# Optimization experiments

Measured on AMD Instinct MI355X. Metric: run time of the kernel, lower is better.

Reference implementation:

```python
import jax, jax.numpy as jnp
import numpy as np
from jax import lax

HIDDEN = 128
HEADS = 2
SR = 4
EPS = 1e-5


def _rope(x, fr, fi):
    # x: (B, h, S, d) ; fr, fi: (S, d//2) broadcast as (1,1,S,c)
    B, H, S, D = x.shape
    x2 = x.reshape(B, H, S, D // 2, 2)
    xr, xi = x2[..., 0], x2[..., 1]
    fr = fr[None, None, :, :]
    fi = fi[None, None, :, :]
    out_r = xr * fr - xi * fi
    out_i = xr * fi + xi * fr
    return jnp.stack([out_r, out_i], axis=-1).reshape(B, H, S, D)


def _layernorm(x, g, b):
    mu = jnp.mean(x, axis=-1, keepdims=True)
    var = jnp.mean(jnp.square(x - mu), axis=-1, keepdims=True)
    return (x - mu) * lax.rsqrt(var + EPS) * g + b


def setup_inputs() -> dict:
    key = jax.random.key(0)
    ks = jax.random.split(key, 12)
    B, S, C = 2, 16384, HIDDEN
    s = 0.02
    return {
        "hidden_states": jax.random.normal(ks[0], (B, S, C), jnp.float32),
        "freqs_cis": jax.random.normal(ks[1], (S, C // HEADS // 2, 2), jnp.float32),
        "Wq": jax.random.normal(ks[2], (C, C), jnp.float32) * s,
        "bq": jnp.zeros((C,), jnp.float32),
        "Wk": jax.random.normal(ks[3], (C, C), jnp.float32) * s,
        "bk": jnp.zeros((C,), jnp.float32),
        "Wv": jax.random.normal(ks[4], (C, C), jnp.float32) * s,
        "bv": jnp.zeros((C,), jnp.float32),
        "W_sr": jax.random.normal(ks[5], (C, C, SR, SR), jnp.float32) * s,  # (O,I,kh,kw)
        "b_sr": jnp.zeros((C,), jnp.float32),
        "ln_g": jnp.ones((C,), jnp.float32),
        "ln_b": jnp.zeros((C,), jnp.float32),
        "height": 128,
        "width": 128,
    }


def reference(hidden_states, freqs_cis, Wq, bq, Wk, bk, Wv, bv, W_sr, b_sr, ln_g, ln_b, height, width):
    B, S, C = hidden_states.shape
    h, d = HEADS, C // HEADS
    c = d // 2

    # query projection on full-resolution tokens
    q = (hidden_states @ Wq.T + bq).reshape(B, S, h, d).transpose(0, 2, 1, 3)  # (B,h,S,d)

    # sequence reduction: conv stride=kernel=SR on (B,C,H,W), then layernorm
    x_img = hidden_states.transpose(0, 2, 1).reshape(B, C, height, width)
    xr = lax.conv_general_dilated(x_img, W_sr, window_strides=(SR, SR), padding="VALID")
    xr = xr + b_sr[None, :, None, None]
    Sk = (height // SR) * (width // SR)
    xr = xr.reshape(B, C, Sk).transpose(0, 2, 1)  # (B, S', C)
    xr = _layernorm(xr, ln_g, ln_b)

    k = (xr @ Wk.T + bk).reshape(B, Sk, h, d).transpose(0, 2, 1, 3)
    v = (xr @ Wv.T + bv).reshape(B, Sk, h, d).transpose(0, 2, 1, 3)

    # RoPE: queries use full freqs; keys use sr-pooled (block-mean) freqs
    fr, fi = freqs_cis[..., 0], freqs_cis[..., 1]  # (S, c)
    q = _rope(q, fr, fi)

    fr_img = fr.reshape(height // SR, SR, width // SR, SR, c).mean(axis=(1, 3))
    fi_img = fi.reshape(height // SR, SR, width // SR, SR, c).mean(axis=(1, 3))
    fr_k = fr_img.reshape(Sk, c)
    fi_k = fi_img.reshape(Sk, c)
    k = _rope(k, fr_k, fi_k)

    scores = jnp.einsum("bhqd,bhkd->bhqk", q, k) / jnp.sqrt(jnp.float32(d))
    probs = jax.nn.softmax(scores, axis=-1)
    ctx = jnp.einsum("bhqk,bhkd->bhqd", probs, v)
    return ctx.transpose(0, 2, 1, 3).reshape(B, S, C)
```

## Files before the change

### kernel.cpp

```cpp
#include <hip/hip_runtime.h>
#include <math.h>

#define B_   2
#define S_   16384
#define SK_  1024
#define IMW_ 128
#define EPS_ 1e-5f

typedef __attribute__((ext_vector_type(8))) short short8v;
typedef __attribute__((ext_vector_type(4))) short short4v;
typedef __attribute__((ext_vector_type(4))) float f32x4;

__device__ __forceinline__ ushort f2bfu(float x) {
    uint u = __float_as_uint(x);
    u += 0x7fffu + ((u >> 16) & 1u);
    return (ushort)(u >> 16);
}
__device__ __forceinline__ uint cvtpk(float a, float b) {
    uint r;
    asm("v_cvt_pk_bf16_f32 %0, %1, %2" : "=v"(r) : "v"(a), "v"(b));
    return r;
}
__device__ __forceinline__ short8v pack8(float4 a, float4 b) {
    union { uint4 u; short8v s; } c;
    c.u = make_uint4(cvtpk(a.x, a.y), cvtpk(a.z, a.w), cvtpk(b.x, b.y), cvtpk(b.z, b.w));
    return c.s;
}

__global__ __launch_bounds__(256) void k_prep(
    const float* __restrict__ Wsr, const float* __restrict__ Wq,
    const float* __restrict__ Wk,  const float* __restrict__ Wv,
    const float* __restrict__ fc,
    ushort* __restrict__ Wsrb, ushort* __restrict__ Wqb,
    ushort* __restrict__ Wkb,  ushort* __restrict__ Wvb,
    float* __restrict__ frk, float* __restrict__ fik)
{
    const int blk = blockIdx.x, t = threadIdx.x;
    if (blk < 64) {
        int i = blk * 256 + t;
        int co = i >> 7, ci = i & 127;
        const float* src = Wsr + (size_t)i * 16;
        float4 v0 = *(const float4*)(src);
        float4 v1 = *(const float4*)(src + 4);
        float4 v2 = *(const float4*)(src + 8);
        float4 v3 = *(const float4*)(src + 12);
        float vv[16] = {v0.x, v0.y, v0.z, v0.w, v1.x, v1.y, v1.z, v1.w,
                        v2.x, v2.y, v2.z, v2.w, v3.x, v3.y, v3.z, v3.w};
        ushort* dst = Wsrb + (size_t)co * 2048 + ci;
        #pragma unroll
        for (int tap = 0; tap < 16; ++tap) dst[tap * 128] = f2bfu(vv[tap]);
    } else if (blk < 88) {
        int seg = (blk - 64) >> 3;
        const float* src = (seg == 0) ? Wq : (seg == 1) ? Wk : Wv;
        ushort* dst = (seg == 0) ? Wqb : (seg == 1) ? Wkb : Wvb;
        int i = ((blk - 64) & 7) * 2048 + t * 8;
        float4 a = *(const float4*)(src + i);
        float4 b = *(const float4*)(src + i + 4);
        *(uint4*)(dst + i) = make_uint4(cvtpk(a.x, a.y), cvtpk(a.z, a.w),
                                        cvtpk(b.x, b.y), cvtpk(b.z, b.w));
    } else {
        int idx = (blk - 88) * 256 + t;
        int c = idx & 31, kk = idx >> 5;
        int y = kk >> 5, x = kk & 31;
        float sr = 0.f, si = 0.f;
        #pragma unroll
        for (int i1 = 0; i1 < 4; ++i1)
            #pragma unroll
            for (int i3 = 0; i3 < 4; ++i3) {
                int s = (4 * y + i1) * IMW_ + 4 * x + i3;
                sr += fc[s * 64 + 2 * c];
                si += fc[s * 64 + 2 * c + 1];
            }
        frk[idx] = sr * 0.0625f;
        fik[idx] = si * 0.0625f;
    }
}

__global__ __launch_bounds__(512) void k_conv(
    const float* __restrict__ hid, const ushort* __restrict__ Wsrb,
    float* __restrict__ partial)
{
    const int t = threadIdx.x;
    const int lane = t & 63, w = t >> 6;
    const int g = lane >> 4, ln = lane & 15;
    const int b = blockIdx.x >> 6, pt = blockIdx.x & 63;
    const int pos = pt * 16 + ln;
    const int y = pos >> 5, x = pos & 31;

    f32x4 acc[8];
    #pragma unroll
    for (int mt = 0; mt < 8; ++mt)
        #pragma unroll
        for (int r = 0; r < 4; ++r) acc[mt][r] = 0.f;

    #pragma unroll
    for (int st = 0; st < 8; ++st) {
        const int tap = 2 * w + (st >> 2);
        const int ci0 = (st & 3) * 32;
        const int ky = tap >> 2, kx = tap & 3;
        const float* hp = hid + ((size_t)b * S_ + (4 * y + ky) * IMW_ + 4 * x + kx) * 128 + ci0 + 8 * g;
        short8v xf = pack8(*(const float4*)hp, *(const float4*)(hp + 4));
        #pragma unroll
        for (int mt = 0; mt < 8; ++mt) {
            short8v wf = *(const short8v*)(Wsrb + (size_t)(16 * mt + ln) * 2048 + tap * 128 + ci0 + 8 * g);
            acc[mt] = __builtin_amdgcn_mfma_f32_16x16x32_bf16(wf, xf, acc[mt], 0, 0, 0);
        }
    }
    float* dst = partial + ((size_t)w * 2048 + b * 1024 + pos) * 128 + 4 * g;
    #pragma unroll
    for (int mt = 0; mt < 8; ++mt)
        *(float4*)(dst + 16 * mt) = make_float4(acc[mt][0], acc[mt][1], acc[mt][2], acc[mt][3]);
}

__global__ __launch_bounds__(256) void k_lnkv(
    const float* __restrict__ partial, const float* __restrict__ bsr,
    const float* __restrict__ lng, const float* __restrict__ lnb,
    const float* __restrict__ FRK, const float* __restrict__ FIK,
    const ushort* __restrict__ Wkb, const ushort* __restrict__ Wvb,
    const float* __restrict__ bk, const float* __restrict__ bv,
    ushort* __restrict__ Kb, ushort* __restrict__ VTb)
{
    __shared__ ushort sXb[16][128];
    const int t = threadIdx.x;
    const int lane = t & 63, w = t >> 6;
    const int g = lane >> 4, ln = lane & 15;
    const int b = blockIdx.x >> 6;
    const int row0 = blockIdx.x * 16;
    const int pos0 = (blockIdx.x & 63) * 16;

    {
        const int row = t >> 4, j0 = (t & 15) * 8;
        float4 b0 = *(const float4*)(bsr + j0);
        float4 b1 = *(const float4*)(bsr + j0 + 4);
        float v[8] = {b0.x, b0.y, b0.z, b0.w, b1.x, b1.y, b1.z, b1.w};
        #pragma unroll
        for (int s = 0; s < 8; ++s) {
            const float* pp = partial + ((size_t)s * 2048 + row0 + row) * 128 + j0;
            float4 a = *(const float4*)pp;
            float4 c = *(const float4*)(pp + 4);
            v[0] += a.x; v[1] += a.y; v[2] += a.z; v[3] += a.w;
            v[4] += c.x; v[5] += c.y; v[6] += c.z; v[7] += c.w;
        }
        float s = v[0] + v[1] + v[2] + v[3] + v[4] + v[5] + v[6] + v[7];
        #pragma unroll
        for (int m = 1; m < 16; m <<= 1) s += __shfl_xor(s, m, 64);
        float mu = s * (1.0f / 128.0f);
        float d[8], vs = 0.f;
        #pragma unroll
        for (int j = 0; j < 8; ++j) { d[j] = v[j] - mu; vs += d[j] * d[j]; }
        #pragma unroll
        for (int m = 1; m < 16; m <<= 1) vs += __shfl_xor(vs, m, 64);
        float rstd = rsqrtf(vs * (1.0f / 128.0f) + EPS_);
        float4 g0 = *(const float4*)(lng + j0);
        float4 g1 = *(const float4*)(lng + j0 + 4);
        float4 c0 = *(const float4*)(lnb + j0);
        float4 c1 = *(const float4*)(lnb + j0 + 4);
        float o[8];
        o[0] = d[0] * rstd * g0.x + c0.x; o[1] = d[1] * rstd * g0.y + c0.y;
        o[2] = d[2] * rstd * g0.z + c0.z; o[3] = d[3] * rstd * g0.w + c0.w;
        o[4] = d[4] * rstd * g1.x + c1.x; o[5] = d[5] * rstd * g1.y + c1.y;
        o[6] = d[6] * rstd * g1.z + c1.z; o[7] = d[7] * rstd * g1.w + c1.w;
        *(uint4*)&sXb[row][j0 ^ ((row & 7) << 3)] =
            make_uint4(cvtpk(o[0], o[1]), cvtpk(o[2], o[3]),
                       cvtpk(o[4], o[5]), cvtpk(o[6], o[7]));
    }
    __syncthreads();

    short8v xn[4];
    #pragma unroll
    for (int ks = 0; ks < 4; ++ks)
        xn[ks] = *(const short8v*)&sXb[ln][(32 * ks + 8 * g) ^ ((ln & 7) << 3)];

    const int h = w & 1;
    const ushort* Wb = (w < 2) ? Wkb : Wvb;
    f32x4 acc2[4];
    #pragma unroll
    for (int mt = 0; mt < 4; ++mt)
        #pragma unroll
        for (int r = 0; r < 4; ++r) acc2[mt][r] = 0.f;
    #pragma unroll
    for (int mt = 0; mt < 4; ++mt)
        #pragma unroll
        for (int ks = 0; ks < 4; ++ks) {
            short8v wf = *(const short8v*)(Wb + (size_t)(64 * h + 16 * mt + ln) * 128 + 32 * ks + 8 * g);
            acc2[mt] = __builtin_amdgcn_mfma_f32_16x16x32_bf16(wf, xn[ks], acc2[mt], 0, 0, 0);
        }

    const int posg = pos0 + ln;
    const int bh = b * 2 + h;
    if (w < 2) {
        #pragma unroll
        for (int mt = 0; mt < 4; ++mt) {
            int col0 = 16 * mt + 4 * g;
            float4 bkv = *(const float4*)(bk + 64 * h + col0);
            float a0 = acc2[mt][0] + bkv.x, a1 = acc2[mt][1] + bkv.y;
            float a2 = acc2[mt][2] + bkv.z, a3 = acc2[mt][3] + bkv.w;
            float2 frv = *(const float2*)(FRK + (size_t)posg * 32 + (col0 >> 1));
            float2 fiv = *(const float2*)(FIK + (size_t)posg * 32 + (col0 >> 1));
            float o0 = a0 * frv.x - a1 * fiv.x;
            float o1 = a0 * fiv.x + a1 * frv.x;
            float o2 = a2 * frv.y - a3 * fiv.y;
            float o3 = a2 * fiv.y + a3 * frv.y;
            *(uint2*)(Kb + ((size_t)bh * SK_ + posg) * 64 + col0) =
                make_uint2(cvtpk(o0, o1), cvtpk(o2, o3));
        }
    } else {
        #pragma unroll
        for (int mt = 0; mt < 4; ++mt) {
            int col0 = 16 * mt + 4 * g;
            float4 bvv = *(const float4*)(bv + 64 * h + col0);
            #pragma unroll
            for (int r = 0; r < 4; ++r)
                VTb[((size_t)bh * 64 + col0 + r) * SK_ + posg] =
                    f2bfu(acc2[mt][r] + (&bvv.x)[r]);
        }
    }
}

__global__ __launch_bounds__(256) void k_attn(
    const float* __restrict__ hid, const ushort* __restrict__ Wqb,
    const float* __restrict__ bq, const float* __restrict__ fc,
    const ushort* __restrict__ Kb, const ushort* __restrict__ VTb,
    float* __restrict__ out)
{
    __shared__ ushort sK[2][64][64];
    __shared__ ushort sV[2][64][64];

    const int t = threadIdx.x;
    const int lane = t & 63, w = t >> 6;
    const int g = lane >> 4, ln = lane & 15;
    const int sbid = (blockIdx.x & 7) * 64 + (blockIdx.x >> 3);
    const int bh = sbid >> 7;
    const int q0b = (sbid & 127) * 128;
    const int b = bh >> 1, h = bh & 1;

    char* sQt = (char*)&sK[0][0][0];

    {
        f32x4 qa[2][4];
        #pragma unroll
        for (int qt = 0; qt < 2; ++qt)
            #pragma unroll
            for (int mt = 0; mt < 4; ++mt)
                #pragma unroll
                for (int r = 0; r < 4; ++r) qa[qt][mt][r] = 0.f;

        #pragma unroll
        for (int ks = 0; ks < 4; ++ks) {
            short8v xf[2];
            #pragma unroll
            for (int qt = 0; qt < 2; ++qt) {
                const float* hp = hid + ((size_t)b * S_ + q0b + w * 32 + 16 * qt + ln) * 128 + 32 * ks + 8 * g;
                xf[qt] = pack8(*(const float4*)hp, *(const float4*)(hp + 4));
            }
            #pragma unroll
            for (int mt = 0; mt < 4; ++mt) {
                short8v wf = *(const short8v*)(Wqb + (size_t)(64 * h + 16 * mt + ln) * 128 + 32 * ks + 8 * g);
                qa[0][mt] = __builtin_amdgcn_mfma_f32_16x16x32_bf16(wf, xf[0], qa[0][mt], 0, 0, 0);
                qa[1][mt] = __builtin_amdgcn_mfma_f32_16x16x32_bf16(wf, xf[1], qa[1][mt], 0, 0, 0);
            }
        }
        const float scale = 0.18033688011112042f;
        #pragma unroll
        for (int qt = 0; qt < 2; ++qt) {
            const int r = w * 32 + 16 * qt + ln;
            const int pos = q0b + r;
            #pragma unroll
            for (int mt = 0; mt < 4; ++mt) {
                int col0 = 16 * mt + 4 * g;
                float4 fv = *(const float4*)(fc + (size_t)pos * 64 + col0);
                float4 bqv = *(const float4*)(bq + 64 * h + col0);
                float a0 = qa[qt][mt][0] + bqv.x, a1 = qa[qt][mt][1] + bqv.y;
                float a2 = qa[qt][mt][2] + bqv.z, a3 = qa[qt][mt][3] + bqv.w;
                float o0 = (a0 * fv.x - a1 * fv.y) * scale;
                float o1 = (a0 * fv.y + a1 * fv.x) * scale;
                float o2 = (a2 * fv.z - a3 * fv.w) * scale;
                float o3 = (a2 * fv.w + a3 * fv.z) * scale;
                int cb = ((col0 >> 3) ^ (r & 7));
                *(uint2*)(sQt + r * 128 + cb * 16 + (g & 1) * 8) =
                    make_uint2(cvtpk(o0, o1), cvtpk(o2, o3));
            }
        }
    }
    short8v qf[2][2];
    #pragma unroll
    for (int qt = 0; qt < 2; ++qt)
        #pragma unroll
        for (int ks = 0; ks < 2; ++ks) {
            const int r = w * 32 + 16 * qt + ln;
            qf[qt][ks] = *(const short8v*)(sQt + r * 128 + (((4 * ks + g) ^ (r & 7)) * 16));
        }
    __syncthreads();

    const int r0 = t >> 3,        m0 = t & 7;
    const int r1 = (t + 256) >> 3, m1 = t & 7;
    const int vA0 = 32 * (m0 >> 2) + 4 * (m0 & 3);
    const int vA1 = 32 * (m1 >> 2) + 4 * (m1 & 3);
    const ushort* kgB = Kb  + (size_t)bh * SK_ * 64;
    const ushort* vgB = VTb + (size_t)bh * 64 * SK_;

    uint4 kb0, kb1, vb0, vb1;
    auto loadCh = [&](int ch) {
        const ushort* kp = kgB + (size_t)ch * 4096;
        kb0 = *(const uint4*)(kp + r0 * 64 + m0 * 8);
        kb1 = *(const uint4*)(kp + r1 * 64 + m1 * 8);
        const ushort* vp = vgB + ch * 64;
        uint2 a0 = *(const uint2*)(vp + (size_t)r0 * SK_ + vA0);
        uint2 b0 = *(const uint2*)(vp + (size_t)r0 * SK_ + vA0 + 16);
        uint2 a1 = *(const uint2*)(vp + (size_t)r1 * SK_ + vA1);
        uint2 b1 = *(const uint2*)(vp + (size_t)r1 * SK_ + vA1 + 16);
        vb0 = make_uint4(a0.x, a0.y, b0.x, b0.y);
        vb1 = make_uint4(a1.x, a1.y, b1.x, b1.y);
    };
    auto writeBuf = [&](int p) {
        char* kd = (char*)&sK[p][0][0];
        char* vd = (char*)&sV[p][0][0];
        *(uint4*)(kd + r0 * 128 + ((m0 ^ (r0 & 7)) * 16)) = kb0;
        *(uint4*)(kd + r1 * 128 + ((m1 ^ (r1 & 7)) * 16)) = kb1;
        *(uint4*)(vd + r0 * 128 + ((m0 ^ (r0 & 7)) * 16)) = vb0;
        *(uint4*)(vd + r1 * 128 + ((m1 ^ (r1 & 7)) * 16)) = vb1;
    };

    f32x4 ctx[2][4];
    #pragma unroll
    for (int qt = 0; qt < 2; ++qt)
        #pragma unroll
        for (int dt = 0; dt < 4; ++dt)
            #pragma unroll
            for (int r = 0; r < 4; ++r) ctx[qt][dt][r] = 0.f;
    float l_run[2] = {0.f, 0.f};

    loadCh(0);
    writeBuf(0);
    loadCh(1);
    __syncthreads();

    for (int ch = 0; ch < 16; ++ch) {
        const int p = ch & 1;
        if (ch < 15) {
            writeBuf(p ^ 1);
            if (ch < 14) loadCh(ch + 2);
        }

        f32x4 sc[4][2];
        #pragma unroll
        for (int kvt = 0; kvt < 4; ++kvt)
            #pragma unroll
            for (int qt = 0; qt < 2; ++qt)
                #pragma unroll
                for (int r = 0; r < 4; ++r) sc[kvt][qt][r] = 0.f;
        #pragma unroll
        for (int ks = 0; ks < 2; ++ks)
            #pragma unroll
            for (int kvt = 0; kvt < 4; ++kvt) {
                const int r = 16 * kvt + ln;
                short8v kf = *(const short8v*)((const char*)&sK[p][0][0] +
                                               r * 128 + (((4 * ks + g) ^ (r & 7)) * 16));
                sc[kvt][0] = __builtin_amdgcn_mfma_f32_16x16x32_bf16(kf, qf[0][ks], sc[kvt][0], 0, 0, 0);
                sc[kvt][1] = __builtin_amdgcn_mfma_f32_16x16x32_bf16(kf, qf[1][ks], sc[kvt][1], 0, 0, 0);
            }

        #pragma unroll
        for (int qt = 0; qt < 2; ++qt)
            #pragma unroll
            for (int kvt = 0; kvt < 4; ++kvt)
                #pragma unroll
                for (int r = 0; r < 4; ++r) {
                    float ev = __builtin_amdgcn_exp2f(sc[kvt][qt][r]);
                    sc[kvt][qt][r] = ev;
                    l_run[qt] += ev;
                }

        #pragma unroll
        for (int ks2 = 0; ks2 < 2; ++ks2) {
            union { uint4 u; short8v s; } pf[2];
            #pragma unroll
            for (int qt = 0; qt < 2; ++qt) {
                pf[qt].u.x = cvtpk(sc[2 * ks2][qt][0],     sc[2 * ks2][qt][1]);
                pf[qt].u.y = cvtpk(sc[2 * ks2][qt][2],     sc[2 * ks2][qt][3]);
                pf[qt].u.z = cvtpk(sc[2 * ks2 + 1][qt][0], sc[2 * ks2 + 1][qt][1]);
                pf[qt].u.w = cvtpk(sc[2 * ks2 + 1][qt][2], sc[2 * ks2 + 1][qt][3]);
            }
            #pragma unroll
            for (int dt = 0; dt < 4; ++dt) {
                const int dd = 16 * dt + ln;
                short8v vf = *(const short8v*)((const char*)&sV[p][0][0] +
                                               dd * 128 + (((4 * ks2 + g) ^ (dd & 7)) * 16));
                ctx[0][dt] = __builtin_amdgcn_mfma_f32_16x16x32_bf16(pf[0].s, vf, ctx[0][dt], 0, 0, 0);
                ctx[1][dt] = __builtin_amdgcn_mfma_f32_16x16x32_bf16(pf[1].s, vf, ctx[1][dt], 0, 0, 0);
            }
        }

        __syncthreads();
    }

    #pragma unroll
    for (int qt = 0; qt < 2; ++qt) {
        float l = l_run[qt];
        l += __shfl_xor(l, 16, 64);
        l += __shfl_xor(l, 32, 64);
        float inv = 1.0f / l;
        #pragma unroll
        for (int r = 0; r < 4; ++r) {
            float ir = __shfl(inv, 4 * g + r, 64);
            int q = q0b + w * 32 + 16 * qt + 4 * g + r;
            float* dst = out + ((size_t)b * S_ + q) * 128 + h * 64;
            #pragma unroll
            for (int dt = 0; dt < 4; ++dt)
                dst[16 * dt + ln] = ctx[qt][dt][r] * ir;
        }
    }
}

extern "C" void kernel_launch(void* const* d_in, const int* in_sizes, int n_in,
                              void* d_out, int out_size, void* d_ws, size_t ws_size,
                              hipStream_t stream) {
    const float* hid = (const float*)d_in[0];
    const float* fc  = (const float*)d_in[1];
    const float* Wq  = (const float*)d_in[2];
    const float* bq  = (const float*)d_in[3];
    const float* Wk  = (const float*)d_in[4];
    const float* bk  = (const float*)d_in[5];
    const float* Wv  = (const float*)d_in[6];
    const float* bv  = (const float*)d_in[7];
    const float* Wsr = (const float*)d_in[8];
    const float* bsr = (const float*)d_in[9];
    const float* lng = (const float*)d_in[10];
    const float* lnb = (const float*)d_in[11];
    float* out = (float*)d_out;

    float* ws = (float*)d_ws;
    float*  partial = ws;
    float*  FRK  = ws + 2097152;
    float*  FIK  = ws + 2129920;
    ushort* Wsrb = (ushort*)(ws + 2162688);
    ushort* Kb   = (ushort*)(ws + 2293760);
    ushort* VTb  = (ushort*)(ws + 2424832);
    ushort* Wqb  = (ushort*)(ws + 2555904);
    ushort* Wkb  = (ushort*)(ws + 2564096);
    ushort* Wvb  = (ushort*)(ws + 2572288);

    k_prep<<<216, 256, 0, stream>>>(Wsr, Wq, Wk, Wv, fc,
                                    Wsrb, Wqb, Wkb, Wvb, FRK, FIK);
    k_conv<<<128, 512, 0, stream>>>(hid, Wsrb, partial);
    k_lnkv<<<128, 256, 0, stream>>>(partial, bsr, lng, lnb, FRK, FIK,
                                    Wkb, Wvb, bk, bv, Kb, VTb);
    k_attn<<<512, 256, 0, stream>>>(hid, Wqb, bq, fc, Kb, VTb, out);
}
```

Measured before the change: 71.94 us.

## Split KV range across warp pairs in attention and merge partial contexts via LDS

Each attention block now handles 64 queries instead of 128, and the grid doubles to 1024 blocks. Waves are paired: each pair shares 32 queries and each wave in the pair processes half of the 1024 keys. The partial contexts and row sums are merged through shared memory at the end. The KV double buffering is replaced by a single buffer holding both halves, with two barriers per iteration. The aim is more parallelism and shorter per-wave loops, at the cost of computing the Q projection once per block for fewer rows, extra synchronisation, and a combine step.

Result: slower. 103.8 us (+44.2%).

```diff
diff --git a/kernel.cpp b/kernel.cpp
--- a/kernel.cpp
+++ b/kernel.cpp
@@ -223,102 +223,99 @@
     const ushort* __restrict__ Kb, const ushort* __restrict__ VTb,
     float* __restrict__ out)
 {
-    __shared__ ushort sK[2][64][64];
-    __shared__ ushort sV[2][64][64];
+    __shared__ ushort sMem[2][2][64][64];
 
     const int t = threadIdx.x;
     const int lane = t & 63, w = t >> 6;
     const int g = lane >> 4, ln = lane & 15;
-    const int sbid = (blockIdx.x & 7) * 64 + (blockIdx.x >> 3);
-    const int bh = sbid >> 7;
-    const int q0b = (sbid & 127) * 128;
+    const int qs = w >> 1, kh = w & 1;
+    const int sbid = (blockIdx.x & 7) * 128 + (blockIdx.x >> 3);
+    const int bh = sbid >> 8;
+    const int q0b = (sbid & 255) * 64;
     const int b = bh >> 1, h = bh & 1;
 
-    char* sQt = (char*)&sK[0][0][0];
+    char* sQt = (char*)&sMem[0][0][0][0];
 
     {
-        f32x4 qa[2][4];
-        #pragma unroll
-        for (int qt = 0; qt < 2; ++qt)
-            #pragma unroll
-            for (int mt = 0; mt < 4; ++mt)
-                #pragma unroll
-                for (int r = 0; r < 4; ++r) qa[qt][mt][r] = 0.f;
+        f32x4 qa[4];
+        #pragma unroll
+        for (int mt = 0; mt < 4; ++mt)
+            #pragma unroll
+            for (int r = 0; r < 4; ++r) qa[mt][r] = 0.f;
 
         #pragma unroll
         for (int ks = 0; ks < 4; ++ks) {
-            short8v xf[2];
-            #pragma unroll
-            for (int qt = 0; qt < 2; ++qt) {
-                const float* hp = hid + ((size_t)b * S_ + q0b + w * 32 + 16 * qt + ln) * 128 + 32 * ks + 8 * g;
-                xf[qt] = pack8(*(const float4*)hp, *(const float4*)(hp + 4));
-            }
+            const float* hp = hid + ((size_t)b * S_ + q0b + w * 16 + ln) * 128 + 32 * ks + 8 * g;
+            short8v xf = pack8(*(const float4*)hp, *(const float4*)(hp + 4));
             #pragma unroll
             for (int mt = 0; mt < 4; ++mt) {
                 short8v wf = *(const short8v*)(Wqb + (size_t)(64 * h + 16 * mt + ln) * 128 + 32 * ks + 8 * g);
-                qa[0][mt] = __builtin_amdgcn_mfma_f32_16x16x32_bf16(wf, xf[0], qa[0][mt], 0, 0, 0);
-                qa[1][mt] = __builtin_amdgcn_mfma_f32_16x16x32_bf16(wf, xf[1], qa[1][mt], 0, 0, 0);
+                qa[mt] = __builtin_amdgcn_mfma_f32_16x16x32_bf16(wf, xf, qa[mt], 0, 0, 0);
             }
         }
         const float scale = 0.18033688011112042f;
-        #pragma unroll
-        for (int qt = 0; qt < 2; ++qt) {
-            const int r = w * 32 + 16 * qt + ln;
-            const int pos = q0b + r;
-            #pragma unroll
-            for (int mt = 0; mt < 4; ++mt) {
-                int col0 = 16 * mt + 4 * g;
-                float4 fv = *(const float4*)(fc + (size_t)pos * 64 + col0);
-                float4 bqv = *(const float4*)(bq + 64 * h + col0);
-                float a0 = qa[qt][mt][0] + bqv.x, a1 = qa[qt][mt][1] + bqv.y;
-                float a2 = qa[qt][mt][2] + bqv.z, a3 = qa[qt][mt][3] + bqv.w;
-                float o0 = (a0 * fv.x - a1 * fv.y) * scale;
-                float o1 = (a0 * fv.y + a1 * fv.x) * scale;
-                float o2 = (a2 * fv.z - a3 * fv.w) * scale;
-                float o3 = (a2 * fv.w + a3 * fv.z) * scale;
-                int cb = ((col0 >> 3) ^ (r & 7));
-                *(uint2*)(sQt + r * 128 + cb * 16 + (g & 1) * 8) =
-                    make_uint2(cvtpk(o0, o1), cvtpk(o2, o3));
-            }
-        }
-    }
+        const int r = w * 16 + ln;
+        const int pos = q0b + r;
+        #pragma unroll
+        for (int mt = 0; mt < 4; ++mt) {
+            int col0 = 16 * mt + 4 * g;
+            float4 fv = *(const float4*)(fc + (size_t)pos * 64 + col0);
+            float4 bqv = *(const float4*)(bq + 64 * h + col0);
+            float a0 = qa[mt][0] + bqv.x, a1 = qa[mt][1] + bqv.y;
+            float a2 = qa[mt][2] + bqv.z, a3 = qa[mt][3] + bqv.w;
+            float o0 = (a0 * fv.x - a1 * fv.y) * scale;
+            float o1 = (a0 * fv.y + a1 * fv.x) * scale;
+            float o2 = (a2 * fv.z - a3 * fv.w) * scale;
+            float o3 = (a2 * fv.w + a3 * fv.z) * scale;
+            int cb = ((col0 >> 3) ^ (r & 7));
+            *(uint2*)(sQt + r * 128 + cb * 16 + (g & 1) * 8) =
+                make_uint2(cvtpk(o0, o1), cvtpk(o2, o3));
+        }
+    }
+    __syncthreads();
+
     short8v qf[2][2];
     #pragma unroll
     for (int qt = 0; qt < 2; ++qt)
         #pragma unroll
         for (int ks = 0; ks < 2; ++ks) {
-            const int r = w * 32 + 16 * qt + ln;
+            const int r = qs * 32 + 16 * qt + ln;
             qf[qt][ks] = *(const short8v*)(sQt + r * 128 + (((4 * ks + g) ^ (r & 7)) * 16));
         }
     __syncthreads();
 
-    const int r0 = t >> 3,        m0 = t & 7;
-    const int r1 = (t + 256) >> 3, m1 = t & 7;
-    const int vA0 = 32 * (m0 >> 2) + 4 * (m0 & 3);
-    const int vA1 = 32 * (m1 >> 2) + 4 * (m1 & 3);
+    const int r0 = t >> 3, m0 = t & 7;
+    const int r1 = r0 + 32;
+    const int vA = 32 * (m0 >> 2) + 4 * (m0 & 3);
     const ushort* kgB = Kb  + (size_t)bh * SK_ * 64;
     const ushort* vgB = VTb + (size_t)bh * 64 * SK_;
 
-    uint4 kb0, kb1, vb0, vb1;
+    uint4 kr[2][2], vr[2][2];
     auto loadCh = [&](int ch) {
-        const ushort* kp = kgB + (size_t)ch * 4096;
-        kb0 = *(const uint4*)(kp + r0 * 64 + m0 * 8);
-        kb1 = *(const uint4*)(kp + r1 * 64 + m1 * 8);
-        const ushort* vp = vgB + ch * 64;
-        uint2 a0 = *(const uint2*)(vp + (size_t)r0 * SK_ + vA0);
-        uint2 b0 = *(const uint2*)(vp + (size_t)r0 * SK_ + vA0 + 16);
-        uint2 a1 = *(const uint2*)(vp + (size_t)r1 * SK_ + vA1);
-        uint2 b1 = *(const uint2*)(vp + (size_t)r1 * SK_ + vA1 + 16);
-        vb0 = make_uint4(a0.x, a0.y, b0.x, b0.y);
-        vb1 = make_uint4(a1.x, a1.y, b1.x, b1.y);
+        #pragma unroll
+        for (int hh = 0; hh < 2; ++hh) {
+            const ushort* kp = kgB + (size_t)(hh * 512 + ch * 64) * 64;
+            kr[hh][0] = *(const uint4*)(kp + r0 * 64 + m0 * 8);
+            kr[hh][1] = *(const uint4*)(kp + r1 * 64 + m0 * 8);
+            const ushort* vp = vgB + hh * 512 + ch * 64;
+            uint2 a0 = *(const uint2*)(vp + (size_t)r0 * SK_ + vA);
+            uint2 b0 = *(const uint2*)(vp + (size_t)r0 * SK_ + vA + 16);
+            uint2 a1 = *(const uint2*)(vp + (size_t)r1 * SK_ + vA);
+            uint2 b1 = *(const uint2*)(vp + (size_t)r1 * SK_ + vA + 16);
+            vr[hh][0] = make_uint4(a0.x, a0.y, b0.x, b0.y);
+            vr[hh][1] = make_uint4(a1.x, a1.y, b1.x, b1.y);
+        }
     };
-    auto writeBuf = [&](int p) {
-        char* kd = (char*)&sK[p][0][0];
-        char* vd = (char*)&sV[p][0][0];
-        *(uint4*)(kd + r0 * 128 + ((m0 ^ (r0 & 7)) * 16)) = kb0;
-        *(uint4*)(kd + r1 * 128 + ((m1 ^ (r1 & 7)) * 16)) = kb1;
-        *(uint4*)(vd + r0 * 128 + ((m0 ^ (r0 & 7)) * 16)) = vb0;
-        *(uint4*)(vd + r1 * 128 + ((m1 ^ (r1 & 7)) * 16)) = vb1;
+    auto writeBuf = [&]() {
+        #pragma unroll
+        for (int hh = 0; hh < 2; ++hh) {
+            char* kd = (char*)&sMem[0][hh][0][0];
+            char* vd = (char*)&sMem[1][hh][0][0];
+            *(uint4*)(kd + r0 * 128 + ((m0 ^ (r0 & 7)) * 16)) = kr[hh][0];
+            *(uint4*)(kd + r1 * 128 + ((m0 ^ (r1 & 7)) * 16)) = kr[hh][1];
+            *(uint4*)(vd + r0 * 128 + ((m0 ^ (r0 & 7)) * 16)) = vr[hh][0];
+            *(uint4*)(vd + r1 * 128 + ((m0 ^ (r1 & 7)) * 16)) = vr[hh][1];
+        }
     };
 
     f32x4 ctx[2][4];
@@ -331,17 +328,11 @@
     float l_run[2] = {0.f, 0.f};
 
     loadCh(0);
-    writeBuf(0);
+    writeBuf();
     loadCh(1);
     __syncthreads();
 
-    for (int ch = 0; ch < 16; ++ch) {
-        const int p = ch & 1;
-        if (ch < 15) {
-            writeBuf(p ^ 1);
-            if (ch < 14) loadCh(ch + 2);
-        }
-
+    for (int ch = 0; ch < 8; ++ch) {
         f32x4 sc[4][2];
         #pragma unroll
         for (int kvt = 0; kvt < 4; ++kvt)
@@ -354,7 +345,7 @@
             #pragma unroll
             for (int kvt = 0; kvt < 4; ++kvt) {
                 const int r = 16 * kvt + ln;
-                short8v kf = *(const short8v*)((const char*)&sK[p][0][0] +
+                short8v kf = *(const short8v*)((const char*)&sMem[0][kh][0][0] +
                                                r * 128 + (((4 * ks + g) ^ (r & 7)) * 16));
                 sc[kvt][0] = __builtin_amdgcn_mfma_f32_16x16x32_bf16(kf, qf[0][ks], sc[kvt][0], 0, 0, 0);
                 sc[kvt][1] = __builtin_amdgcn_mfma_f32_16x16x32_bf16(kf, qf[1][ks], sc[kvt][1], 0, 0, 0);
@@ -384,7 +375,7 @@
             #pragma unroll
             for (int dt = 0; dt < 4; ++dt) {
                 const int dd = 16 * dt + ln;
-                short8v vf = *(const short8v*)((const char*)&sV[p][0][0] +
+                short8v vf = *(const short8v*)((const char*)&sMem[1][kh][0][0] +
                                                dd * 128 + (((4 * ks2 + g) ^ (dd & 7)) * 16));
                 ctx[0][dt] = __builtin_amdgcn_mfma_f32_16x16x32_bf16(pf[0].s, vf, ctx[0][dt], 0, 0, 0);
                 ctx[1][dt] = __builtin_amdgcn_mfma_f32_16x16x32_bf16(pf[1].s, vf, ctx[1][dt], 0, 0, 0);
@@ -392,22 +383,48 @@
         }
 
         __syncthreads();
+        if (ch < 7) writeBuf();
+        if (ch < 6) loadCh(ch + 2);
+        __syncthreads();
     }
 
     #pragma unroll
     for (int qt = 0; qt < 2; ++qt) {
-        float l = l_run[qt];
-        l += __shfl_xor(l, 16, 64);
-        l += __shfl_xor(l, 32, 64);
-        float inv = 1.0f / l;
-        #pragma unroll
-        for (int r = 0; r < 4; ++r) {
-            float ir = __shfl(inv, 4 * g + r, 64);
-            int q = q0b + w * 32 + 16 * qt + 4 * g + r;
-            float* dst = out + ((size_t)b * S_ + q) * 128 + h * 64;
+        l_run[qt] += __shfl_xor(l_run[qt], 16, 64);
+        l_run[qt] += __shfl_xor(l_run[qt], 32, 64);
+    }
+
+    float* scr = (float*)&sMem[0][0][0][0];
+    if (kh == 1) {
+        float* dst = scr + (size_t)(qs * 64 + lane) * 35;
+        #pragma unroll
+        for (int qt = 0; qt < 2; ++qt)
             #pragma unroll
             for (int dt = 0; dt < 4; ++dt)
-                dst[16 * dt + ln] = ctx[qt][dt][r] * ir;
+                #pragma unroll
+                for (int r = 0; r < 4; ++r)
+                    dst[qt * 16 + dt * 4 + r] = ctx[qt][dt][r];
+        dst[32] = l_run[0];
+        dst[33] = l_run[1];
+    }
+    __syncthreads();
+
+    if (kh == 0) {
+        const float* src = scr + (size_t)(qs * 64 + lane) * 35;
+        float inv0 = 1.0f / (l_run[0] + src[32]);
+        float inv1 = 1.0f / (l_run[1] + src[33]);
+        #pragma unroll
+        for (int qt = 0; qt < 2; ++qt) {
+            float inv = qt ? inv1 : inv0;
+            #pragma unroll
+            for (int r = 0; r < 4; ++r) {
+                float ir = __shfl(inv, 4 * g + r, 64);
+                int q = q0b + qs * 32 + 16 * qt + 4 * g + r;
+                float* dst = out + ((size_t)b * S_ + q) * 128 + h * 64;
+                #pragma unroll
+                for (int dt = 0; dt < 4; ++dt)
+                    dst[16 * dt + ln] = (ctx[qt][dt][r] + src[qt * 16 + dt * 4 + r]) * ir;
+            }
         }
     }
 }
@@ -445,5 +462,5 @@
     k_conv<<<128, 512, 0, stream>>>(hid, Wsrb, partial);
     k_lnkv<<<128, 256, 0, stream>>>(partial, bsr, lng, lnb, FRK, FIK,
                                     Wkb, Wvb, bk, bv, Kb, VTb);
-    k_attn<<<512, 256, 0, stream>>>(hid, Wqb, bq, fc, Kb, VTb, out);
-}
+    k_attn<<<1024, 256, 0, stream>>>(hid, Wqb, bq, fc, Kb, VTb, out);
+}
```

## Fuse SR conv with layernorm and K/V projection into one kernel

Applied to the files above, without the earlier changes.

Merges the strided conv kernel and the layernorm+K/V projection kernel into a single kernel. Each block now handles 4 reduced positions across all 128 output channels, staging the input patches through double-buffered LDS. This removes the 8-way split-K partial buffer write/read and one launch. In exchange, 3/4 of the MFMA lanes compute padding (only 4 of 16 columns are valid), and the layernorm variance is now computed as E[x^2]-mu^2, which is less numerically robust. The grid grows to 512 blocks, and each block re-reads the full conv weight.

New measurement: 79.84 us. +11.0%, slower.

```diff
diff --git a/kernel.cpp b/kernel.cpp
--- a/kernel.cpp
+++ b/kernel.cpp
@@ -76,100 +76,101 @@
     }
 }
 
-__global__ __launch_bounds__(512) void k_conv(
+__global__ __launch_bounds__(256) void k_cvkv(
     const float* __restrict__ hid, const ushort* __restrict__ Wsrb,
-    float* __restrict__ partial)
+    const float* __restrict__ bsr, const float* __restrict__ lng,
+    const float* __restrict__ lnb, const float* __restrict__ FRK,
+    const float* __restrict__ FIK, const ushort* __restrict__ Wkb,
+    const ushort* __restrict__ Wvb, const float* __restrict__ bk,
+    const float* __restrict__ bv, ushort* __restrict__ Kb,
+    ushort* __restrict__ VTb)
 {
+    __shared__ ushort sP[2][4][512];
+    __shared__ ushort sXb[4][128];
+    __shared__ float  sRed[2][4][16];
+
     const int t = threadIdx.x;
     const int lane = t & 63, w = t >> 6;
     const int g = lane >> 4, ln = lane & 15;
-    const int b = blockIdx.x >> 6, pt = blockIdx.x & 63;
-    const int pos = pt * 16 + ln;
-    const int y = pos >> 5, x = pos & 31;
-
-    f32x4 acc[8];
-    #pragma unroll
-    for (int mt = 0; mt < 8; ++mt)
-        #pragma unroll
-        for (int r = 0; r < 4; ++r) acc[mt][r] = 0.f;
-
-    #pragma unroll
-    for (int st = 0; st < 8; ++st) {
-        const int tap = 2 * w + (st >> 2);
-        const int ci0 = (st & 3) * 32;
-        const int ky = tap >> 2, kx = tap & 3;
-        const float* hp = hid + ((size_t)b * S_ + (4 * y + ky) * IMW_ + 4 * x + kx) * 128 + ci0 + 8 * g;
-        short8v xf = pack8(*(const float4*)hp, *(const float4*)(hp + 4));
-        #pragma unroll
-        for (int mt = 0; mt < 8; ++mt) {
-            short8v wf = *(const short8v*)(Wsrb + (size_t)(16 * mt + ln) * 2048 + tap * 128 + ci0 + 8 * g);
-            acc[mt] = __builtin_amdgcn_mfma_f32_16x16x32_bf16(wf, xf, acc[mt], 0, 0, 0);
-        }
-    }
-    float* dst = partial + ((size_t)w * 2048 + b * 1024 + pos) * 128 + 4 * g;
-    #pragma unroll
-    for (int mt = 0; mt < 8; ++mt)
-        *(float4*)(dst + 16 * mt) = make_float4(acc[mt][0], acc[mt][1], acc[mt][2], acc[mt][3]);
-}
-
-__global__ __launch_bounds__(256) void k_lnkv(
-    const float* __restrict__ partial, const float* __restrict__ bsr,
-    const float* __restrict__ lng, const float* __restrict__ lnb,
-    const float* __restrict__ FRK, const float* __restrict__ FIK,
-    const ushort* __restrict__ Wkb, const ushort* __restrict__ Wvb,
-    const float* __restrict__ bk, const float* __restrict__ bv,
-    ushort* __restrict__ Kb, ushort* __restrict__ VTb)
-{
-    __shared__ ushort sXb[16][128];
-    const int t = threadIdx.x;
-    const int lane = t & 63, w = t >> 6;
-    const int g = lane >> 4, ln = lane & 15;
-    const int b = blockIdx.x >> 6;
-    const int row0 = blockIdx.x * 16;
-    const int pos0 = (blockIdx.x & 63) * 16;
-
-    {
-        const int row = t >> 4, j0 = (t & 15) * 8;
-        float4 b0 = *(const float4*)(bsr + j0);
-        float4 b1 = *(const float4*)(bsr + j0 + 4);
-        float v[8] = {b0.x, b0.y, b0.z, b0.w, b1.x, b1.y, b1.z, b1.w};
-        #pragma unroll
-        for (int s = 0; s < 8; ++s) {
-            const float* pp = partial + ((size_t)s * 2048 + row0 + row) * 128 + j0;
-            float4 a = *(const float4*)pp;
-            float4 c = *(const float4*)(pp + 4);
-            v[0] += a.x; v[1] += a.y; v[2] += a.z; v[3] += a.w;
-            v[4] += c.x; v[5] += c.y; v[6] += c.z; v[7] += c.w;
-        }
-        float s = v[0] + v[1] + v[2] + v[3] + v[4] + v[5] + v[6] + v[7];
-        #pragma unroll
-        for (int m = 1; m < 16; m <<= 1) s += __shfl_xor(s, m, 64);
-        float mu = s * (1.0f / 128.0f);
-        float d[8], vs = 0.f;
-        #pragma unroll
-        for (int j = 0; j < 8; ++j) { d[j] = v[j] - mu; vs += d[j] * d[j]; }
-        #pragma unroll
-        for (int m = 1; m < 16; m <<= 1) vs += __shfl_xor(vs, m, 64);
-        float rstd = rsqrtf(vs * (1.0f / 128.0f) + EPS_);
-        float4 g0 = *(const float4*)(lng + j0);
-        float4 g1 = *(const float4*)(lng + j0 + 4);
-        float4 c0 = *(const float4*)(lnb + j0);
-        float4 c1 = *(const float4*)(lnb + j0 + 4);
-        float o[8];
-        o[0] = d[0] * rstd * g0.x + c0.x; o[1] = d[1] * rstd * g0.y + c0.y;
-        o[2] = d[2] * rstd * g0.z + c0.z; o[3] = d[3] * rstd * g0.w + c0.w;
-        o[4] = d[4] * rstd * g1.x + c1.x; o[5] = d[5] * rstd * g1.y + c1.y;
-        o[6] = d[6] * rstd * g1.z + c1.z; o[7] = d[7] * rstd * g1.w + c1.w;
-        *(uint4*)&sXb[row][j0 ^ ((row & 7) << 3)] =
-            make_uint4(cvtpk(o[0], o[1]), cvtpk(o[2], o[3]),
-                       cvtpk(o[4], o[5]), cvtpk(o[6], o[7]));
-    }
+    const int rowg = blockIdx.x * 4;
+    const int b = rowg >> 10;
+    const int posB = rowg & 1023;
+
+    const int sp = t >> 6;
+    const int su = t & 63;
+    auto stage = [&](int c, int buf) {
+        int tap = c * 4 + (su >> 4);
+        int ci  = (su & 15) * 8;
+        int pg  = posB + sp;
+        int y = pg >> 5, x = pg & 31;
+        const float* hp = hid + ((size_t)b * S_ + (4 * y + (tap >> 2)) * IMW_ + 4 * x + (tap & 3)) * 128 + ci;
+        short8v v = pack8(*(const float4*)hp, *(const float4*)(hp + 4));
+        *(short8v*)&sP[buf][sp][(su ^ (sp & 3)) * 8] = v;
+    };
+
+    f32x4 acc[2];
+    #pragma unroll
+    for (int m = 0; m < 2; ++m)
+        #pragma unroll
+        for (int r = 0; r < 4; ++r) acc[m][r] = 0.f;
+
+    stage(0, 0);
     __syncthreads();
+    for (int c = 0; c < 4; ++c) {
+        if (c < 3) stage(c + 1, (c + 1) & 1);
+        const int bf = c & 1;
+        #pragma unroll
+        for (int ksl = 0; ksl < 16; ++ksl) {
+            short8v xf = *(const short8v*)&sP[bf][ln & 3][(((4 * ksl + g) ^ (ln & 3))) * 8];
+            int kg = c * 512 + ksl * 32 + 8 * g;
+            #pragma unroll
+            for (int m = 0; m < 2; ++m) {
+                short8v wf = *(const short8v*)(Wsrb + (size_t)(32 * w + 16 * m + ln) * 2048 + kg);
+                acc[m] = __builtin_amdgcn_mfma_f32_16x16x32_bf16(wf, xf, acc[m], 0, 0, 0);
+            }
+        }
+        __syncthreads();
+    }
+
+    float ps = 0.f, pq = 0.f;
+    #pragma unroll
+    for (int m = 0; m < 2; ++m) {
+        float4 bs = *(const float4*)(bsr + 32 * w + 16 * m + 4 * g);
+        #pragma unroll
+        for (int r = 0; r < 4; ++r) {
+            acc[m][r] += (&bs.x)[r];
+            ps += acc[m][r];
+            pq += acc[m][r] * acc[m][r];
+        }
+    }
+    ps += __shfl_xor(ps, 16, 64); ps += __shfl_xor(ps, 32, 64);
+    pq += __shfl_xor(pq, 16, 64); pq += __shfl_xor(pq, 32, 64);
+    if (lane < 16) { sRed[0][w][ln] = ps; sRed[1][w][ln] = pq; }
+    __syncthreads();
+    float s4 = sRed[0][0][ln] + sRed[0][1][ln] + sRed[0][2][ln] + sRed[0][3][ln];
+    float q4 = sRed[1][0][ln] + sRed[1][1][ln] + sRed[1][2][ln] + sRed[1][3][ln];
+    float mu = s4 * (1.0f / 128.0f);
+    float rstd = rsqrtf(fmaxf(q4 * (1.0f / 128.0f) - mu * mu, 0.f) + EPS_);
+
+    #pragma unroll
+    for (int m = 0; m < 2; ++m) {
+        int co0 = 32 * w + 16 * m + 4 * g;
+        float4 gg = *(const float4*)(lng + co0);
+        float4 bb = *(const float4*)(lnb + co0);
+        float o0 = (acc[m][0] - mu) * rstd * gg.x + bb.x;
+        float o1 = (acc[m][1] - mu) * rstd * gg.y + bb.y;
+        float o2 = (acc[m][2] - mu) * rstd * gg.z + bb.z;
+        float o3 = (acc[m][3] - mu) * rstd * gg.w + bb.w;
+        int U = co0 >> 3, half = g & 1, p = ln & 3;
+        *(uint2*)((char*)&sXb[0][0] + p * 256 + ((U ^ p) * 16) + half * 8) =
+            make_uint2(cvtpk(o0, o1), cvtpk(o2, o3));
+    }
+    __syncthreads();
 
     short8v xn[4];
     #pragma unroll
     for (int ks = 0; ks < 4; ++ks)
-        xn[ks] = *(const short8v*)&sXb[ln][(32 * ks + 8 * g) ^ ((ln & 7) << 3)];
+        xn[ks] = *(const short8v*)((char*)&sXb[0][0] + (ln & 3) * 256 + (((4 * ks + g) ^ (ln & 3)) * 16));
 
     const int h = w & 1;
     const ushort* Wb = (w < 2) ? Wkb : Wvb;
@@ -186,33 +187,35 @@
             acc2[mt] = __builtin_amdgcn_mfma_f32_16x16x32_bf16(wf, xn[ks], acc2[mt], 0, 0, 0);
         }
 
-    const int posg = pos0 + ln;
-    const int bh = b * 2 + h;
-    if (w < 2) {
-        #pragma unroll
-        for (int mt = 0; mt < 4; ++mt) {
-            int col0 = 16 * mt + 4 * g;
-            float4 bkv = *(const float4*)(bk + 64 * h + col0);
-            float a0 = acc2[mt][0] + bkv.x, a1 = acc2[mt][1] + bkv.y;
-            float a2 = acc2[mt][2] + bkv.z, a3 = acc2[mt][3] + bkv.w;
-            float2 frv = *(const float2*)(FRK + (size_t)posg * 32 + (col0 >> 1));
-            float2 fiv = *(const float2*)(FIK + (size_t)posg * 32 + (col0 >> 1));
-            float o0 = a0 * frv.x - a1 * fiv.x;
-            float o1 = a0 * fiv.x + a1 * frv.x;
-            float o2 = a2 * frv.y - a3 * fiv.y;
-            float o3 = a2 * fiv.y + a3 * frv.y;
-            *(uint2*)(Kb + ((size_t)bh * SK_ + posg) * 64 + col0) =
-                make_uint2(cvtpk(o0, o1), cvtpk(o2, o3));
-        }
-    } else {
-        #pragma unroll
-        for (int mt = 0; mt < 4; ++mt) {
-            int col0 = 16 * mt + 4 * g;
-            float4 bvv = *(const float4*)(bv + 64 * h + col0);
-            #pragma unroll
-            for (int r = 0; r < 4; ++r)
-                VTb[((size_t)bh * 64 + col0 + r) * SK_ + posg] =
-                    f2bfu(acc2[mt][r] + (&bvv.x)[r]);
+    if (ln < 4) {
+        const int posg = posB + ln;
+        const int bh = b * 2 + h;
+        if (w < 2) {
+            #pragma unroll
+            for (int mt = 0; mt < 4; ++mt) {
+                int col0 = 16 * mt + 4 * g;
+                float4 bkv = *(const float4*)(bk + 64 * h + col0);
+                float a0 = acc2[mt][0] + bkv.x, a1 = acc2[mt][1] + bkv.y;
+                float a2 = acc2[mt][2] + bkv.z, a3 = acc2[mt][3] + bkv.w;
+                float2 frv = *(const float2*)(FRK + (size_t)posg * 32 + (col0 >> 1));
+                float2 fiv = *(const float2*)(FIK + (size_t)posg * 32 + (col0 >> 1));
+                float o0 = a0 * frv.x - a1 * fiv.x;
+                float o1 = a0 * fiv.x + a1 * frv.x;
+                float o2 = a2 * frv.y - a3 * fiv.y;
+                float o3 = a2 * fiv.y + a3 * frv.y;
+                *(uint2*)(Kb + ((size_t)bh * SK_ + posg) * 64 + col0) =
+                    make_uint2(cvtpk(o0, o1), cvtpk(o2, o3));
+            }
+        } else {
+            #pragma unroll
+            for (int mt = 0; mt < 4; ++mt) {
+                int col0 = 16 * mt + 4 * g;
+                float4 bvv = *(const float4*)(bv + 64 * h + col0);
+                #pragma unroll
+                for (int r = 0; r < 4; ++r)
+                    VTb[((size_t)bh * 64 + col0 + r) * SK_ + posg] =
+                        f2bfu(acc2[mt][r] + (&bvv.x)[r]);
+            }
         }
     }
 }
@@ -430,7 +433,6 @@
     float* out = (float*)d_out;
 
     float* ws = (float*)d_ws;
-    float*  partial = ws;
     float*  FRK  = ws + 2097152;
     float*  FIK  = ws + 2129920;
     ushort* Wsrb = (ushort*)(ws + 2162688);
@@ -442,8 +444,7 @@
 
     k_prep<<<216, 256, 0, stream>>>(Wsr, Wq, Wk, Wv, fc,
                                     Wsrb, Wqb, Wkb, Wvb, FRK, FIK);
-    k_conv<<<128, 512, 0, stream>>>(hid, Wsrb, partial);
-    k_lnkv<<<128, 256, 0, stream>>>(partial, bsr, lng, lnb, FRK, FIK,
+    k_cvkv<<<512, 256, 0, stream>>>(hid, Wsrb, bsr, lng, lnb, FRK, FIK,
                                     Wkb, Wvb, bk, bv, Kb, VTb);
     k_attn<<<512, 256, 0, stream>>>(hid, Wqb, bq, fc, Kb, VTb, out);
 }
```

## Fold weight bf16 conversion and pooled RoPE freqs into consumer kernels

Applied to the files above, without the earlier changes.

Shrinks the prep kernel to only the conv-weight reorder. Pooled key RoPE frequencies are now computed in shared memory inside the LN/KV kernel, and Wq/Wk/Wv are converted from fp32 to bf16 at load time in their consumer kernels. This cuts the prep kernel's grid and removes the workspace round trip for those buffers. It also adds s_setprio raises around the MFMA blocks in attention. The cost is twice the fp32 weight traffic plus redundant conversions in every attention block.

Result: slower. 77.41 us (+7.6%).

```diff
diff --git a/kernel.cpp b/kernel.cpp
--- a/kernel.cpp
+++ b/kernel.cpp
@@ -27,53 +27,20 @@
     return c.s;
 }
 
-__global__ __launch_bounds__(256) void k_prep(
-    const float* __restrict__ Wsr, const float* __restrict__ Wq,
-    const float* __restrict__ Wk,  const float* __restrict__ Wv,
-    const float* __restrict__ fc,
-    ushort* __restrict__ Wsrb, ushort* __restrict__ Wqb,
-    ushort* __restrict__ Wkb,  ushort* __restrict__ Wvb,
-    float* __restrict__ frk, float* __restrict__ fik)
-{
-    const int blk = blockIdx.x, t = threadIdx.x;
-    if (blk < 64) {
-        int i = blk * 256 + t;
-        int co = i >> 7, ci = i & 127;
-        const float* src = Wsr + (size_t)i * 16;
-        float4 v0 = *(const float4*)(src);
-        float4 v1 = *(const float4*)(src + 4);
-        float4 v2 = *(const float4*)(src + 8);
-        float4 v3 = *(const float4*)(src + 12);
-        float vv[16] = {v0.x, v0.y, v0.z, v0.w, v1.x, v1.y, v1.z, v1.w,
-                        v2.x, v2.y, v2.z, v2.w, v3.x, v3.y, v3.z, v3.w};
-        ushort* dst = Wsrb + (size_t)co * 2048 + ci;
-        #pragma unroll
-        for (int tap = 0; tap < 16; ++tap) dst[tap * 128] = f2bfu(vv[tap]);
-    } else if (blk < 88) {
-        int seg = (blk - 64) >> 3;
-        const float* src = (seg == 0) ? Wq : (seg == 1) ? Wk : Wv;
-        ushort* dst = (seg == 0) ? Wqb : (seg == 1) ? Wkb : Wvb;
-        int i = ((blk - 64) & 7) * 2048 + t * 8;
-        float4 a = *(const float4*)(src + i);
-        float4 b = *(const float4*)(src + i + 4);
-        *(uint4*)(dst + i) = make_uint4(cvtpk(a.x, a.y), cvtpk(a.z, a.w),
-                                        cvtpk(b.x, b.y), cvtpk(b.z, b.w));
-    } else {
-        int idx = (blk - 88) * 256 + t;
-        int c = idx & 31, kk = idx >> 5;
-        int y = kk >> 5, x = kk & 31;
-        float sr = 0.f, si = 0.f;
-        #pragma unroll
-        for (int i1 = 0; i1 < 4; ++i1)
-            #pragma unroll
-            for (int i3 = 0; i3 < 4; ++i3) {
-                int s = (4 * y + i1) * IMW_ + 4 * x + i3;
-                sr += fc[s * 64 + 2 * c];
-                si += fc[s * 64 + 2 * c + 1];
-            }
-        frk[idx] = sr * 0.0625f;
-        fik[idx] = si * 0.0625f;
-    }
+__global__ __launch_bounds__(256) void k_prep(const float* __restrict__ Wsr,
+                                              ushort* __restrict__ Wsrb) {
+    int i = blockIdx.x * 256 + threadIdx.x;
+    int co = i >> 7, ci = i & 127;
+    const float* src = Wsr + (size_t)i * 16;
+    float4 v0 = *(const float4*)(src);
+    float4 v1 = *(const float4*)(src + 4);
+    float4 v2 = *(const float4*)(src + 8);
+    float4 v3 = *(const float4*)(src + 12);
+    float vv[16] = {v0.x, v0.y, v0.z, v0.w, v1.x, v1.y, v1.z, v1.w,
+                    v2.x, v2.y, v2.z, v2.w, v3.x, v3.y, v3.z, v3.w};
+    ushort* dst = Wsrb + (size_t)co * 2048 + ci;
+    #pragma unroll
+    for (int tap = 0; tap < 16; ++tap) dst[tap * 128] = f2bfu(vv[tap]);
 }
 
 __global__ __launch_bounds__(512) void k_conv(
@@ -115,18 +82,39 @@
 __global__ __launch_bounds__(256) void k_lnkv(
     const float* __restrict__ partial, const float* __restrict__ bsr,
     const float* __restrict__ lng, const float* __restrict__ lnb,
-    const float* __restrict__ FRK, const float* __restrict__ FIK,
-    const ushort* __restrict__ Wkb, const ushort* __restrict__ Wvb,
+    const float* __restrict__ fc,
+    const float* __restrict__ Wk, const float* __restrict__ Wv,
     const float* __restrict__ bk, const float* __restrict__ bv,
     ushort* __restrict__ Kb, ushort* __restrict__ VTb)
 {
     __shared__ ushort sXb[16][128];
+    __shared__ float  sFR[16][32];
+    __shared__ float  sFI[16][32];
     const int t = threadIdx.x;
     const int lane = t & 63, w = t >> 6;
     const int g = lane >> 4, ln = lane & 15;
     const int b = blockIdx.x >> 6;
     const int row0 = blockIdx.x * 16;
     const int pos0 = (blockIdx.x & 63) * 16;
+
+    #pragma unroll
+    for (int i = 0; i < 2; ++i) {
+        int pid = t + 256 * i;
+        int p = pid >> 5, c = pid & 31;
+        int pg = pos0 + p;
+        int y = pg >> 5, x = pg & 31;
+        float sr = 0.f, si = 0.f;
+        #pragma unroll
+        for (int i1 = 0; i1 < 4; ++i1)
+            #pragma unroll
+            for (int i3 = 0; i3 < 4; ++i3) {
+                int s = (4 * y + i1) * IMW_ + 4 * x + i3;
+                sr += fc[s * 64 + 2 * c];
+                si += fc[s * 64 + 2 * c + 1];
+            }
+        sFR[p][c] = sr * 0.0625f;
+        sFI[p][c] = si * 0.0625f;
+    }
 
     {
         const int row = t >> 4, j0 = (t & 15) * 8;
@@ -172,7 +160,7 @@
         xn[ks] = *(const short8v*)&sXb[ln][(32 * ks + 8 * g) ^ ((ln & 7) << 3)];
 
     const int h = w & 1;
-    const ushort* Wb = (w < 2) ? Wkb : Wvb;
+    const float* W = (w < 2) ? Wk : Wv;
     f32x4 acc2[4];
     #pragma unroll
     for (int mt = 0; mt < 4; ++mt)
@@ -182,7 +170,8 @@
     for (int mt = 0; mt < 4; ++mt)
         #pragma unroll
         for (int ks = 0; ks < 4; ++ks) {
-            short8v wf = *(const short8v*)(Wb + (size_t)(64 * h + 16 * mt + ln) * 128 + 32 * ks + 8 * g);
+            const float* wp = W + (size_t)(64 * h + 16 * mt + ln) * 128 + 32 * ks + 8 * g;
+            short8v wf = pack8(*(const float4*)wp, *(const float4*)(wp + 4));
             acc2[mt] = __builtin_amdgcn_mfma_f32_16x16x32_bf16(wf, xn[ks], acc2[mt], 0, 0, 0);
         }
 
@@ -195,8 +184,8 @@
             float4 bkv = *(const float4*)(bk + 64 * h + col0);
             float a0 = acc2[mt][0] + bkv.x, a1 = acc2[mt][1] + bkv.y;
             float a2 = acc2[mt][2] + bkv.z, a3 = acc2[mt][3] + bkv.w;
-            float2 frv = *(const float2*)(FRK + (size_t)posg * 32 + (col0 >> 1));
-            float2 fiv = *(const float2*)(FIK + (size_t)posg * 32 + (col0 >> 1));
+            float2 frv = *(const float2*)&sFR[ln][col0 >> 1];
+            float2 fiv = *(const float2*)&sFI[ln][col0 >> 1];
             float o0 = a0 * frv.x - a1 * fiv.x;
             float o1 = a0 * fiv.x + a1 * frv.x;
             float o2 = a2 * frv.y - a3 * fiv.y;
@@ -218,7 +207,7 @@
 }
 
 __global__ __launch_bounds__(256) void k_attn(
-    const float* __restrict__ hid, const ushort* __restrict__ Wqb,
+    const float* __restrict__ hid, const float* __restrict__ Wq,
     const float* __restrict__ bq, const float* __restrict__ fc,
     const ushort* __restrict__ Kb, const ushort* __restrict__ VTb,
     float* __restrict__ out)
@@ -255,7 +244,8 @@
             }
             #pragma unroll
             for (int mt = 0; mt < 4; ++mt) {
-                short8v wf = *(const short8v*)(Wqb + (size_t)(64 * h + 16 * mt + ln) * 128 + 32 * ks + 8 * g);
+                const float* wp = Wq + (size_t)(64 * h + 16 * mt + ln) * 128 + 32 * ks + 8 * g;
+                short8v wf = pack8(*(const float4*)wp, *(const float4*)(wp + 4));
                 qa[0][mt] = __builtin_amdgcn_mfma_f32_16x16x32_bf16(wf, xf[0], qa[0][mt], 0, 0, 0);
                 qa[1][mt] = __builtin_amdgcn_mfma_f32_16x16x32_bf16(wf, xf[1], qa[1][mt], 0, 0, 0);
             }
@@ -349,6 +339,7 @@
             for (int qt = 0; qt < 2; ++qt)
                 #pragma unroll
                 for (int r = 0; r < 4; ++r) sc[kvt][qt][r] = 0.f;
+        __builtin_amdgcn_s_setprio(1);
         #pragma unroll
         for (int ks = 0; ks < 2; ++ks)
             #pragma unroll
@@ -359,6 +350,7 @@
                 sc[kvt][0] = __builtin_amdgcn_mfma_f32_16x16x32_bf16(kf, qf[0][ks], sc[kvt][0], 0, 0, 0);
                 sc[kvt][1] = __builtin_amdgcn_mfma_f32_16x16x32_bf16(kf, qf[1][ks], sc[kvt][1], 0, 0, 0);
             }
+        __builtin_amdgcn_s_setprio(0);
 
         #pragma unroll
         for (int qt = 0; qt < 2; ++qt)
@@ -381,6 +373,7 @@
                 pf[qt].u.z = cvtpk(sc[2 * ks2 + 1][qt][0], sc[2 * ks2 + 1][qt][1]);
                 pf[qt].u.w = cvtpk(sc[2 * ks2 + 1][qt][2], sc[2 * ks2 + 1][qt][3]);
             }
+            __builtin_amdgcn_s_setprio(1);
             #pragma unroll
             for (int dt = 0; dt < 4; ++dt) {
                 const int dd = 16 * dt + ln;
@@ -389,6 +382,7 @@
                 ctx[0][dt] = __builtin_amdgcn_mfma_f32_16x16x32_bf16(pf[0].s, vf, ctx[0][dt], 0, 0, 0);
                 ctx[1][dt] = __builtin_amdgcn_mfma_f32_16x16x32_bf16(pf[1].s, vf, ctx[1][dt], 0, 0, 0);
             }
+            __builtin_amdgcn_s_setprio(0);
         }
 
         __syncthreads();
@@ -431,19 +425,13 @@
 
     float* ws = (float*)d_ws;
     float*  partial = ws;
-    float*  FRK  = ws + 2097152;
-    float*  FIK  = ws + 2129920;
-    ushort* Wsrb = (ushort*)(ws + 2162688);
-    ushort* Kb   = (ushort*)(ws + 2293760);
-    ushort* VTb  = (ushort*)(ws + 2424832);
-    ushort* Wqb  = (ushort*)(ws + 2555904);
-    ushort* Wkb  = (ushort*)(ws + 2564096);
-    ushort* Wvb  = (ushort*)(ws + 2572288);
-
-    k_prep<<<216, 256, 0, stream>>>(Wsr, Wq, Wk, Wv, fc,
-                                    Wsrb, Wqb, Wkb, Wvb, FRK, FIK);
+    ushort* Wsrb = (ushort*)(ws + 2097152);
+    ushort* Kb   = (ushort*)(ws + 2228224);
+    ushort* VTb  = (ushort*)(ws + 2359296);
+
+    k_prep<<<64, 256, 0, stream>>>(Wsr, Wsrb);
     k_conv<<<128, 512, 0, stream>>>(hid, Wsrb, partial);
-    k_lnkv<<<128, 256, 0, stream>>>(partial, bsr, lng, lnb, FRK, FIK,
-                                    Wkb, Wvb, bk, bv, Kb, VTb);
-    k_attn<<<512, 256, 0, stream>>>(hid, Wqb, bq, fc, Kb, VTb, out);
-}
+    k_lnkv<<<128, 256, 0, stream>>>(partial, bsr, lng, lnb, fc,
+                                    Wk, Wv, bk, bv, Kb, VTb);
+    k_attn<<<512, 256, 0, stream>>>(hid, Wq, bq, fc, Kb, VTb, out);
+}
```
